# Optimization experiments

Measured on AMD Instinct MI355X. Metric: run time of the kernel, lower is better.

## Reference

```python
import jax, jax.numpy as jnp
import numpy as np

EPS = 1e-3  # tfa InstanceNormalization default epsilon
H = 4       # num_attention_heads


def _inorm(x, g, b, axes):
    # instance norm: normalize over the given (spatial) axes, affine per channel
    m = jnp.mean(x, axis=axes, keepdims=True)
    v = jnp.var(x, axis=axes, keepdims=True)
    return (x - m) * jax.lax.rsqrt(v + EPS) * g + b


def setup_inputs() -> dict:
    key = jax.random.key(0)
    ks = jax.random.split(key, 20)
    B, N, C, E = 1, 196, 480, 4  # batch, tokens, KV_size_C, embedding_channels
    d = {}
    for i, n in enumerate(['emb1', 'emb2', 'emb3', 'emb4']):
        d[n] = jax.random.normal(ks[i], (B, N, E), jnp.float32)
    d['emb_C'] = jax.random.normal(ks[4], (B, N, C), jnp.float32)
    for i, n in enumerate(['Wq_C', 'Wk_C', 'Wv_C']):
        d[n] = jax.random.normal(ks[5 + i], (C, C), jnp.float32) * 0.02
    for i, n in enumerate(['Wq1', 'Wq2', 'Wq3', 'Wq4', 'Wk', 'Wv', 'Wo1', 'Wo2', 'Wo3', 'Wo4']):
        d[n] = jax.random.normal(ks[8 + i], (E, E), jnp.float32) * 0.25
    d['g1'] = jnp.ones((), jnp.float32)   # psi1 gamma (single channel)
    d['b1'] = jnp.zeros((), jnp.float32)  # psi1 beta
    d['g2'] = jnp.ones((H,), jnp.float32)   # psi2 gamma (per head)
    d['b2'] = jnp.zeros((H,), jnp.float32)  # psi2 beta
    return d


def reference(emb1, emb2, emb3, emb4, emb_C, Wq_C, Wk_C, Wv_C,
              Wq1, Wq2, Wq3, Wq4, Wk, Wv, Wo1, Wo2, Wo3, Wo4,
              g1, b1, g2, b2):
    B, N, C = emb_C.shape
    # ---- channel attention over emb_C ----
    Qc = emb_C @ Wq_C
    Kc = emb_C @ Wk_C
    Vc = emb_C @ Wv_C
    attn = jnp.einsum('bnc,bnd->bcd', Qc, Kc)            # Q_C^T @ K_C  [B,C,C]
    attn = _inorm(attn, g1, b1, axes=(-2, -1))           # psi1: 1-channel instance norm
    sim = jax.nn.softmax(attn, axis=-1)                  # dropout inactive (inference)
    T_hat = jnp.einsum('bcd,bnd->bnc', sim, Vc)          # (sim @ V_C^T)^T  [B,N,C]
    # split into C//4 chunks of width 4 along channels, concat along tokens
    KV_S = T_hat.reshape(B, N, C // 4, 4).transpose(0, 2, 1, 3).reshape(B, (C // 4) * N, 4)

    def heads(x):  # [B,T,4] -> [B,H,T,1]
        return x.reshape(B, -1, H, 1).transpose(0, 2, 1, 3)

    K = heads(KV_S @ Wk)   # [B,H,M,1], M = N*C//4
    V = heads(KV_S @ Wv)
    gh = g2.reshape(1, H, 1, 1)
    bh = b2.reshape(1, H, 1, 1)

    def branch(emb, Wq, Wo):
        Q = heads(emb @ Wq)                                  # [B,H,Nq,1]
        a = jnp.einsum('bhqd,bhkd->bhqk', Q, K)              # [B,H,Nq,M]
        a = _inorm(a, gh, bh, axes=(-2, -1))                 # psi2: per-head instance norm
        a = jax.nn.softmax(a, axis=-1)
        c = jnp.einsum('bhqk,bhkd->bhqd', a, V)              # [B,H,Nq,1]
        c = c.transpose(0, 2, 1, 3).reshape(B, -1, H)        # [B,Nq,4] (= KV_size_S)
        return c @ Wo

    return (branch(emb1, Wq1, Wo1), branch(emb2, Wq2, Wo2),
            branch(emb3, Wq3, Wo3), branch(emb4, Wq4, Wo4))
```

## Files before the change

### kernel.cpp

```cpp
#include <hip/hip_runtime.h>
#include <hip/hip_bf16.h>
#include <math.h>

#define N_TOK 196
#define M_KV  23520
#define EPSN  1e-3f
#define LOG2E 1.44269504088896340736f

#define OFF_QC    0
#define OFF_KC    94080
#define OFF_VC    188160
#define OFF_ATTN  282240
#define OFF_KV    512640
#define OFF_SPART 700800
#define OFF_KPART 701056

__device__ __forceinline__ float fast_exp2(float x) {
#if __has_builtin(__builtin_amdgcn_exp2f)
    return __builtin_amdgcn_exp2f(x);
#else
    return exp2f(x);
#endif
}

#define GEMM_COMPUTE(AS, BS) \
    _Pragma("unroll") \
    for (int kk2 = 0; kk2 < 16; ++kk2) { \
        float4 av = *(const float4*)&AS[kk2][ty*4]; \
        float2 bv = *(const float2*)&BS[kk2][tx*2]; \
        a00 = fmaf(av.x, bv.x, a00); a01 = fmaf(av.x, bv.y, a01); \
        a10 = fmaf(av.y, bv.x, a10); a11 = fmaf(av.y, bv.y, a11); \
        a20 = fmaf(av.z, bv.x, a20); a21 = fmaf(av.z, bv.y, a21); \
        a30 = fmaf(av.w, bv.x, a30); a31 = fmaf(av.w, bv.y, a31); \
    }

#define COMBINE_ACCS(CMB) \
    if (kg == 1) { \
        CMB[ty*4+0][tx*2] = a00; CMB[ty*4+0][tx*2+1] = a01; \
        CMB[ty*4+1][tx*2] = a10; CMB[ty*4+1][tx*2+1] = a11; \
        CMB[ty*4+2][tx*2] = a20; CMB[ty*4+2][tx*2+1] = a21; \
        CMB[ty*4+3][tx*2] = a30; CMB[ty*4+3][tx*2+1] = a31; \
    } \
    __syncthreads(); \
    if (kg == 0) { \
        a00 += CMB[ty*4+0][tx*2]; a01 += CMB[ty*4+0][tx*2+1]; \
        a10 += CMB[ty*4+1][tx*2]; a11 += CMB[ty*4+1][tx*2+1]; \
        a20 += CMB[ty*4+2][tx*2]; a21 += CMB[ty*4+2][tx*2+1]; \
        a30 += CMB[ty*4+3][tx*2]; a31 += CMB[ty*4+3][tx*2+1]; \
    }

__global__ __launch_bounds__(512) void k_qkv(const float* __restrict__ embC,
                                             const float* __restrict__ Wq,
                                             const float* __restrict__ Wk,
                                             const float* __restrict__ Wv,
                                             float* __restrict__ ws) {
    int bid = blockIdx.x;
    int zi = bid / 60, rem = bid % 60;
    int m0 = (rem / 15) * 64, n0 = (rem % 15) * 32;
    const float* W = (zi == 0) ? Wq : (zi == 1 ? Wk : Wv);
    float* o = ws + zi * 94080;
    __shared__ float As[2][2][16][68];
    __shared__ float Bs[2][2][16][36];
    __shared__ float Cmb[64][33];
    int tid = threadIdx.x;
    int kg = tid >> 8, t = tid & 255;
    int ty = t >> 4, tx = t & 15;
    float a00=0,a01=0,a10=0,a11=0,a20=0,a21=0,a30=0,a31=0;
    const float4 z4 = make_float4(0,0,0,0);
    int mrow = t >> 2, kq = (t & 3) * 4;
    bool am = (m0 + mrow) < N_TOK;
    const float* aptr = embC + (m0 + mrow) * 480 + kg * 240 + kq;
    bool bact = t < 128;
    int kk = t >> 3, nq = (t & 7) * 4;
    const float* bptr = W + (kg * 240 + kk) * 480 + n0 + nq;
    const int NS = 15;
    float4 ra = am ? *(const float4*)(aptr) : z4;
    float4 rb = bact ? *(const float4*)(bptr) : z4;
    As[kg][0][kq+0][mrow]=ra.x; As[kg][0][kq+1][mrow]=ra.y;
    As[kg][0][kq+2][mrow]=ra.z; As[kg][0][kq+3][mrow]=ra.w;
    if (bact) *(float4*)&Bs[kg][0][kk][nq] = rb;
    ra = am ? *(const float4*)(aptr + 16) : z4;
    rb = bact ? *(const float4*)(bptr + 16*480) : z4;
    __syncthreads();
    for (int s = 0; s < NS; ++s) {
        int b = s & 1;
        float4 fa = z4, fb = z4;
        if (s + 2 < NS) {
            fa = am ? *(const float4*)(aptr + (s+2)*16) : z4;
            fb = bact ? *(const float4*)(bptr + (s+2)*16*480) : z4;
        }
        GEMM_COMPUTE(As[kg][b], Bs[kg][b]);
        if (s + 1 < NS) {
            int nb = b ^ 1;
            As[kg][nb][kq+0][mrow]=ra.x; As[kg][nb][kq+1][mrow]=ra.y;
            As[kg][nb][kq+2][mrow]=ra.z; As[kg][nb][kq+3][mrow]=ra.w;
            if (bact) *(float4*)&Bs[kg][nb][kk][nq] = rb;
        }
        __syncthreads();
        ra = fa; rb = fb;
    }
    COMBINE_ACCS(Cmb);
    if (kg == 0) {
        int m = m0 + ty*4, n = n0 + tx*2;
        if (m   < N_TOK) *(float2*)(o + (m  )*480 + n) = make_float2(a00, a01);
        if (m+1 < N_TOK) *(float2*)(o + (m+1)*480 + n) = make_float2(a10, a11);
        if (m+2 < N_TOK) *(float2*)(o + (m+2)*480 + n) = make_float2(a20, a21);
        if (m+3 < N_TOK) *(float2*)(o + (m+3)*480 + n) = make_float2(a30, a31);
    }
}

__global__ __launch_bounds__(512) void k_attn(const float* __restrict__ Qc,
                                              const float* __restrict__ Kc,
                                              float* __restrict__ attn,
                                              float* __restrict__ Spart) {
    __shared__ float As[2][2][16][68];
    __shared__ float Bs[2][2][16][36];
    __shared__ float Cmb[64][33];
    __shared__ float red[8][2];
    int tid = threadIdx.x;
    int kg = tid >> 8, t = tid & 255;
    int n0 = blockIdx.x * 32, m0 = blockIdx.y * 64;
    int ty = t >> 4, tx = t & 15;
    float a00=0,a01=0,a10=0,a11=0,a20=0,a21=0,a30=0,a31=0;
    const float4 z4 = make_float4(0,0,0,0);
    int kka = t >> 4, mq = (t & 15) * 4;
    bool amq = (m0 + mq) < 480;
    int kbase = kg * 112;
    const float* aptr = Qc + (kbase + kka) * 480 + m0 + mq;
    bool bact = t < 128;
    int kk = t >> 3, nq = (t & 7) * 4;
    const float* bptr = Kc + (kbase + kk) * 480 + n0 + nq;
    const int NS = 7;
    float4 ra = (amq && kbase + kka < N_TOK) ? *(const float4*)(aptr) : z4;
    float4 rb = (bact && kbase + kk < N_TOK) ? *(const float4*)(bptr) : z4;
    *(float4*)&As[kg][0][kka][mq] = ra;
    if (bact) *(float4*)&Bs[kg][0][kk][nq] = rb;
    ra = (amq && kbase + 16 + kka < N_TOK) ? *(const float4*)(aptr + 16*480) : z4;
    rb = (bact && kbase + 16 + kk < N_TOK) ? *(const float4*)(bptr + 16*480) : z4;
    __syncthreads();
    for (int s = 0; s < NS; ++s) {
        int b = s & 1;
        float4 fa = z4, fb = z4;
        if (s + 2 < NS) {
            int k0 = kbase + (s + 2) * 16;
            fa = (amq && k0 + kka < N_TOK) ? *(const float4*)(aptr + (s+2)*16*480) : z4;
            fb = (bact && k0 + kk < N_TOK) ? *(const float4*)(bptr + (s+2)*16*480) : z4;
        }
        GEMM_COMPUTE(As[kg][b], Bs[kg][b]);
        if (s + 1 < NS) {
            int nb = b ^ 1;
            *(float4*)&As[kg][nb][kka][mq] = ra;
            if (bact) *(float4*)&Bs[kg][nb][kk][nq] = rb;
        }
        __syncthreads();
        ra = fa; rb = fb;
    }
    COMBINE_ACCS(Cmb);
    float ls = 0.f, lq = 0.f;
    if (kg == 0) {
        int m = m0 + ty*4, n = n0 + tx*2;
        if (m   < 480) *(float2*)(attn + (m  )*480 + n) = make_float2(a00, a01);
        if (m+1 < 480) *(float2*)(attn + (m+1)*480 + n) = make_float2(a10, a11);
        if (m+2 < 480) *(float2*)(attn + (m+2)*480 + n) = make_float2(a20, a21);
        if (m+3 < 480) *(float2*)(attn + (m+3)*480 + n) = make_float2(a30, a31);
        ls = a00+a01+a10+a11+a20+a21+a30+a31;
        lq = a00*a00+a01*a01+a10*a10+a11*a11+a20*a20+a21*a21+a30*a30+a31*a31;
    }
    #pragma unroll
    for (int o = 32; o > 0; o >>= 1) { ls += __shfl_xor(ls, o, 64); lq += __shfl_xor(lq, o, 64); }
    int wid = tid >> 6, lane = tid & 63;
    if (lane == 0) { red[wid][0] = ls; red[wid][1] = lq; }
    __syncthreads();
    if (tid == 0) {
        int bid = blockIdx.y * gridDim.x + blockIdx.x;
        Spart[bid*2]   = red[0][0] + red[1][0] + red[2][0] + red[3][0];
        Spart[bid*2+1] = red[0][1] + red[1][1] + red[2][1] + red[3][1];
    }
}

__global__ __launch_bounds__(512) void k_thatkv(const float* __restrict__ Vc,
                                                const float* __restrict__ attn,
                                                const float* __restrict__ Spart,
                                                const float* __restrict__ g1,
                                                const float* __restrict__ Wk,
                                                const float* __restrict__ Wv,
                                                float2* __restrict__ KV,
                                                float* __restrict__ kpart) {
    __shared__ float As[2][2][16][68];
    __shared__ float Bs[2][2][16][36];
    __shared__ float red[8][16];
    __shared__ float colsum[32];
    __shared__ float Tile[64][33];
    int bid = blockIdx.x;
    int n0 = (bid % 15) * 32, m0 = (bid / 15) * 64;
    int tid = threadIdx.x;
    int kg = tid >> 8, t = tid & 255;
    int wid = tid >> 6, lane = tid & 63;
    if (tid < 32) colsum[tid] = 0.f;
    float ps = 0.f, pq = 0.f;
    if (tid < 120) { ps = Spart[tid*2]; pq = Spart[tid*2+1]; }
    #pragma unroll
    for (int o = 32; o > 0; o >>= 1) { ps += __shfl_xor(ps, o, 64); pq += __shfl_xor(pq, o, 64); }
    if (lane == 0) { red[wid][0] = ps; red[wid][1] = pq; }
    __syncthreads();
    float S = 0.f, SQ = 0.f;
    #pragma unroll
    for (int w = 0; w < 8; ++w) { S += red[w][0]; SQ += red[w][1]; }
    const float invCC = 1.f / (480.f * 480.f);
    float mean = S * invCC;
    float var  = SQ * invCC - mean * mean;
    float s2 = g1[0] * rsqrtf(var + EPSN) * LOG2E;
    int ty = t >> 4, tx = t & 15;
    float a00=0,a01=0,a10=0,a11=0,a20=0,a21=0,a30=0,a31=0;
    const float4 z4 = make_float4(0,0,0,0);
    int mrow = t >> 2, kq = (t & 3) * 4;
    bool am = (m0 + mrow) < N_TOK;
    const float* aptr = Vc + (m0 + mrow) * 480 + kg * 240 + kq;
    bool bact = t < 128;
    int nrow = t >> 2, bkq = (t & 3) * 4;
    const float* bptr = attn + (n0 + nrow) * 480 + kg * 240 + bkq;
    float bsum = 0.f;
    const int NS = 15;
    float4 ra = am ? *(const float4*)(aptr) : z4;
    float4 rb = bact ? *(const float4*)(bptr) : z4;
    As[kg][0][kq+0][mrow]=ra.x; As[kg][0][kq+1][mrow]=ra.y;
    As[kg][0][kq+2][mrow]=ra.z; As[kg][0][kq+3][mrow]=ra.w;
    if (bact) {
        float e0 = fast_exp2(s2 * rb.x), e1 = fast_exp2(s2 * rb.y);
        float e2 = fast_exp2(s2 * rb.z), e3 = fast_exp2(s2 * rb.w);
        Bs[kg][0][bkq+0][nrow] = e0; Bs[kg][0][bkq+1][nrow] = e1;
        Bs[kg][0][bkq+2][nrow] = e2; Bs[kg][0][bkq+3][nrow] = e3;
        bsum += e0 + e1 + e2 + e3;
    }
    ra = am ? *(const float4*)(aptr + 16) : z4;
    rb = bact ? *(const float4*)(bptr + 16) : z4;
    __syncthreads();
    for (int s = 0; s < NS; ++s) {
        int b = s & 1;
        float4 fa = z4, fb = z4;
        if (s + 2 < NS) {
            fa = am ? *(const float4*)(aptr + (s+2)*16) : z4;
            fb = bact ? *(const float4*)(bptr + (s+2)*16) : z4;
        }
        GEMM_COMPUTE(As[kg][b], Bs[kg][b]);
        if (s + 1 < NS) {
            int nb = b ^ 1;
            As[kg][nb][kq+0][mrow]=ra.x; As[kg][nb][kq+1][mrow]=ra.y;
            As[kg][nb][kq+2][mrow]=ra.z; As[kg][nb][kq+3][mrow]=ra.w;
            if (bact) {
                float e0 = fast_exp2(s2 * rb.x), e1 = fast_exp2(s2 * rb.y);
                float e2 = fast_exp2(s2 * rb.z), e3 = fast_exp2(s2 * rb.w);
                Bs[kg][nb][bkq+0][nrow] = e0; Bs[kg][nb][bkq+1][nrow] = e1;
                Bs[kg][nb][bkq+2][nrow] = e2; Bs[kg][nb][bkq+3][nrow] = e3;
                bsum += e0 + e1 + e2 + e3;
            }
        }
        __syncthreads();
        ra = fa; rb = fb;
    }
    if (bact) atomicAdd(&colsum[nrow], bsum);
    __syncthreads();
    if (tid < 32) colsum[tid] = 1.f / colsum[tid];
    int r0 = ty*4, cc = tx*2;
    if (kg == 1) {
        Tile[r0+0][cc] = a00; Tile[r0+0][cc+1] = a01;
        Tile[r0+1][cc] = a10; Tile[r0+1][cc+1] = a11;
        Tile[r0+2][cc] = a20; Tile[r0+2][cc+1] = a21;
        Tile[r0+3][cc] = a30; Tile[r0+3][cc+1] = a31;
    }
    __syncthreads();
    if (kg == 0) {
        float i0 = colsum[cc], i1 = colsum[cc+1];
        Tile[r0+0][cc] = (Tile[r0+0][cc] + a00) * i0; Tile[r0+0][cc+1] = (Tile[r0+0][cc+1] + a01) * i1;
        Tile[r0+1][cc] = (Tile[r0+1][cc] + a10) * i0; Tile[r0+1][cc+1] = (Tile[r0+1][cc+1] + a11) * i1;
        Tile[r0+2][cc] = (Tile[r0+2][cc] + a20) * i0; Tile[r0+2][cc+1] = (Tile[r0+2][cc+1] + a21) * i1;
        Tile[r0+3][cc] = (Tile[r0+3][cc] + a30) * i0; Tile[r0+3][cc+1] = (Tile[r0+3][cc+1] + a31) * i1;
    }
    __syncthreads();
    float su[4] = {0,0,0,0}, sq[4] = {0,0,0,0};
    {
        int e = tid;
        int tr = e >> 3, jj = e & 7;
        int tok = m0 + tr;
        bool act = tok < N_TOK;
        float c0 = Tile[tr][4*jj], c1 = Tile[tr][4*jj+1];
        float c2 = Tile[tr][4*jj+2], c3 = Tile[tr][4*jj+3];
        int m_kv = (n0/4 + jj) * 196 + tok;
        #pragma unroll
        for (int h = 0; h < 4; ++h) {
            float kh = c0*Wk[h] + c1*Wk[4+h] + c2*Wk[8+h] + c3*Wk[12+h];
            float vh = c0*Wv[h] + c1*Wv[4+h] + c2*Wv[8+h] + c3*Wv[12+h];
            if (act) {
                KV[h * M_KV + m_kv] = make_float2(kh, vh);
                su[h] += kh; sq[h] += kh * kh;
            }
        }
    }
    __syncthreads();
    #pragma unroll
    for (int h = 0; h < 4; ++h) {
        #pragma unroll
        for (int o = 32; o > 0; o >>= 1) {
            su[h] += __shfl_xor(su[h], o, 64);
            sq[h] += __shfl_xor(sq[h], o, 64);
        }
        if (lane == 0) { red[wid][h*2+0] = su[h]; red[wid][h*2+1] = sq[h]; }
    }
    __syncthreads();
    if (tid < 8) {
        int h = tid & 3, st = tid >> 2;
        float r = 0.f;
        #pragma unroll
        for (int w = 0; w < 8; ++w) r += red[w][h*2+st];
        kpart[st * 256 + h * 64 + bid] = r;
    }
}

#define QG 49
__global__ __launch_bounds__(1024) void k_branch(
        const float* __restrict__ emb1, const float* __restrict__ emb2,
        const float* __restrict__ emb3, const float* __restrict__ emb4,
        const float* __restrict__ Wq1, const float* __restrict__ Wq2,
        const float* __restrict__ Wq3, const float* __restrict__ Wq4,
        const float* __restrict__ g2v,
        const float2* __restrict__ KV, const float* __restrict__ kpart,
        const float* __restrict__ Wo1, const float* __restrict__ Wo2,
        const float* __restrict__ Wo3, const float* __restrict__ Wo4,
        float* __restrict__ out) {
    __shared__ float lsh[4][4][4];
    __shared__ float ash[4][4][4];
    int tid = threadIdx.x;
    int w = tid >> 6, lane = tid & 63;
    int h = w >> 2, p = w & 3;
    int bid = blockIdx.x;
    int i = bid / QG, qg = bid % QG;
    const float* emb = (i == 0) ? emb1 : (i == 1) ? emb2 : (i == 2) ? emb3 : emb4;
    const float* Wq  = (i == 0) ? Wq1 : (i == 1) ? Wq2 : (i == 2) ? Wq3 : Wq4;
    float wq0 = Wq[h], wq1 = Wq[4+h], wq2 = Wq[8+h], wq3 = Wq[12+h];
    float s = 0.f, s2 = 0.f;
    #pragma unroll
    for (int r = 0; r < 4; ++r) {
        int t = lane + r * 64;
        if (t < N_TOK) {
            float Q = emb[t*4]*wq0 + emb[t*4+1]*wq1 + emb[t*4+2]*wq2 + emb[t*4+3]*wq3;
            s += Q; s2 += Q * Q;
        }
    }
    float ks = 0.f, kq2 = 0.f;
    if (lane < 60) {
        ks  = kpart[0*256 + h*64 + lane];
        kq2 = kpart[1*256 + h*64 + lane];
    }
    #pragma unroll
    for (int o = 32; o > 0; o >>= 1) {
        s += __shfl_xor(s, o, 64); s2 += __shfl_xor(s2, o, 64);
        ks += __shfl_xor(ks, o, 64); kq2 += __shfl_xor(kq2, o, 64);
    }
    float Qbar = s * (1.f/196.f), Q2bar = s2 * (1.f/196.f);
    float Kbar = ks * (1.f/(float)M_KV), K2bar = kq2 * (1.f/(float)M_KV);
    float mu = Qbar * Kbar;
    float var = Q2bar * K2bar - mu * mu;
    float sc = g2v[h] * rsqrtf(var + EPSN);
    float B2[4];
    #pragma unroll
    for (int j = 0; j < 4; ++j) {
        int q = qg * 4 + j;
        float Qj = emb[q*4]*wq0 + emb[q*4+1]*wq1 + emb[q*4+2]*wq2 + emb[q*4+3]*wq3;
        B2[j] = Qj * sc * LOG2E;
    }
    const float4* kv4 = (const float4*)(KV + h * M_KV);
    const int KQ = M_KV / 8;
    int kstart = p * KQ, kendq = kstart + KQ;
    float l[4] = {0,0,0,0};
    float a[4] = {0,0,0,0};
#define PROC8(P) { \
        _Pragma("unroll") \
        for (int j = 0; j < 4; ++j) { \
            float x = fast_exp2(B2[j] * P.x); \
            l[j] += x; a[j] = fmaf(x, P.y, a[j]); \
            float y = fast_exp2(B2[j] * P.z); \
            l[j] += y; a[j] = fmaf(y, P.w, a[j]); \
        } }
    int k4 = kstart + lane;
    for (; k4 + 192 < kendq; k4 += 256) {
        float4 p0 = kv4[k4], p1 = kv4[k4+64], p2 = kv4[k4+128], p3 = kv4[k4+192];
        PROC8(p0); PROC8(p1); PROC8(p2); PROC8(p3);
    }
    for (; k4 < kendq; k4 += 64) { float4 pv = kv4[k4]; PROC8(pv); }
#undef PROC8
    #pragma unroll
    for (int j = 0; j < 4; ++j) {
        float lv = l[j], av = a[j];
        #pragma unroll
        for (int o = 32; o > 0; o >>= 1) { lv += __shfl_xor(lv, o, 64); av += __shfl_xor(av, o, 64); }
        if (lane == 0) { lsh[h][p][j] = lv; ash[h][p][j] = av; }
    }
    __syncthreads();
    if (tid < 4) {
        const float* Wo = (i == 0) ? Wo1 : (i == 1) ? Wo2 : (i == 2) ? Wo3 : Wo4;
        int j = tid;
        float c[4];
        #pragma unroll
        for (int hh = 0; hh < 4; ++hh) {
            float L = lsh[hh][0][j] + lsh[hh][1][j] + lsh[hh][2][j] + lsh[hh][3][j];
            float A = ash[hh][0][j] + ash[hh][1][j] + ash[hh][2][j] + ash[hh][3][j];
            c[hh] = A / L;
        }
        float4 o;
        o.x = c[0]*Wo[0] + c[1]*Wo[4] + c[2]*Wo[8]  + c[3]*Wo[12];
        o.y = c[0]*Wo[1] + c[1]*Wo[5] + c[2]*Wo[9]  + c[3]*Wo[13];
        o.z = c[0]*Wo[2] + c[1]*Wo[6] + c[2]*Wo[10] + c[3]*Wo[14];
        o.w = c[0]*Wo[3] + c[1]*Wo[7] + c[2]*Wo[11] + c[3]*Wo[15];
        *(float4*)(out + i * 784 + (qg * 4 + j) * 4) = o;
    }
}

extern "C" void kernel_launch(void* const* d_in, const int* in_sizes, int n_in,
                              void* d_out, int out_size, void* d_ws, size_t ws_size,
                              hipStream_t stream) {
    const float* emb1 = (const float*)d_in[0];
    const float* emb2 = (const float*)d_in[1];
    const float* emb3 = (const float*)d_in[2];
    const float* emb4 = (const float*)d_in[3];
    const float* embC = (const float*)d_in[4];
    const float* WqC  = (const float*)d_in[5];
    const float* WkC  = (const float*)d_in[6];
    const float* WvC  = (const float*)d_in[7];
    const float* Wq1  = (const float*)d_in[8];
    const float* Wq2  = (const float*)d_in[9];
    const float* Wq3  = (const float*)d_in[10];
    const float* Wq4  = (const float*)d_in[11];
    const float* Wk   = (const float*)d_in[12];
    const float* Wv   = (const float*)d_in[13];
    const float* Wo1  = (const float*)d_in[14];
    const float* Wo2  = (const float*)d_in[15];
    const float* Wo3  = (const float*)d_in[16];
    const float* Wo4  = (const float*)d_in[17];
    const float* g1   = (const float*)d_in[18];
    const float* g2   = (const float*)d_in[20];
    float* ws = (float*)d_ws;
    float* out = (float*)d_out;

    k_qkv<<<180, 512, 0, stream>>>(embC, WqC, WkC, WvC, ws);
    k_attn<<<dim3(15, 8), 512, 0, stream>>>(ws + OFF_QC, ws + OFF_KC,
                                            ws + OFF_ATTN, ws + OFF_SPART);
    k_thatkv<<<60, 512, 0, stream>>>(ws + OFF_VC, ws + OFF_ATTN, ws + OFF_SPART, g1,
                                     Wk, Wv, (float2*)(ws + OFF_KV), ws + OFF_KPART);
    k_branch<<<4 * QG, 1024, 0, stream>>>(emb1, emb2, emb3, emb4,
                                          Wq1, Wq2, Wq3, Wq4, g2,
                                          (const float2*)(ws + OFF_KV), ws + OFF_KPART,
                                          Wo1, Wo2, Wo3, Wo4, out);
}
```

Before: 64.87 us.

## Fuse four kernels into one persistent kernel with grid-wide atomic barriers

Measured after the change: 95.21 us. +46.8%, slower.

```diff
diff --git a/kernel.cpp b/kernel.cpp
--- a/kernel.cpp
+++ b/kernel.cpp
@@ -6,6 +6,7 @@
 #define M_KV  23520
 #define EPSN  1e-3f
 #define LOG2E 1.44269504088896340736f
+#define NB    256
 
 #define OFF_QC    0
 #define OFF_KC    94080
@@ -14,6 +15,7 @@
 #define OFF_KV    512640
 #define OFF_SPART 700800
 #define OFF_KPART 701056
+#define OFF_SYNC  702080
 
 __device__ __forceinline__ float fast_exp2(float x) {
 #if __has_builtin(__builtin_amdgcn_exp2f)
@@ -21,6 +23,31 @@
 #else
     return exp2f(x);
 #endif
+}
+
+__device__ __forceinline__ void gsync(unsigned* sy, int phase, int bid) {
+    __syncthreads();
+    if (threadIdx.x == 0) {
+        __builtin_amdgcn_fence(__ATOMIC_RELEASE, "agent");
+        unsigned* grp  = sy + phase * 16 + (bid >> 4);
+        unsigned* glob = sy + 128 + phase;
+        unsigned* go   = sy + 144 + phase * 16;
+        if (__hip_atomic_fetch_add(grp, 1u, __ATOMIC_RELAXED, __HIP_MEMORY_SCOPE_AGENT) == 15u) {
+            if (__hip_atomic_fetch_add(glob, 1u, __ATOMIC_RELAXED, __HIP_MEMORY_SCOPE_AGENT) == 15u) {
+                __hip_atomic_store(go, 1u, __ATOMIC_RELAXED, __HIP_MEMORY_SCOPE_AGENT);
+            }
+        }
+        int it = 0;
+        while (__hip_atomic_load(go, __ATOMIC_RELAXED, __HIP_MEMORY_SCOPE_AGENT) == 0u) {
+            if (it < 2)      __builtin_amdgcn_s_sleep(1);
+            else if (it < 4) __builtin_amdgcn_s_sleep(4);
+            else if (it < 8) __builtin_amdgcn_s_sleep(16);
+            else             __builtin_amdgcn_s_sleep(32);
+            ++it;
+        }
+        __builtin_amdgcn_fence(__ATOMIC_ACQUIRE, "agent");
+    }
+    __syncthreads();
 }
 
 #define GEMM_COMPUTE(AS, BS) \
@@ -34,345 +61,341 @@
         a30 = fmaf(av.w, bv.x, a30); a31 = fmaf(av.w, bv.y, a31); \
     }
 
-#define COMBINE_ACCS(CMB) \
-    if (kg == 1) { \
-        CMB[ty*4+0][tx*2] = a00; CMB[ty*4+0][tx*2+1] = a01; \
-        CMB[ty*4+1][tx*2] = a10; CMB[ty*4+1][tx*2+1] = a11; \
-        CMB[ty*4+2][tx*2] = a20; CMB[ty*4+2][tx*2+1] = a21; \
-        CMB[ty*4+3][tx*2] = a30; CMB[ty*4+3][tx*2+1] = a31; \
-    } \
-    __syncthreads(); \
-    if (kg == 0) { \
-        a00 += CMB[ty*4+0][tx*2]; a01 += CMB[ty*4+0][tx*2+1]; \
-        a10 += CMB[ty*4+1][tx*2]; a11 += CMB[ty*4+1][tx*2+1]; \
-        a20 += CMB[ty*4+2][tx*2]; a21 += CMB[ty*4+2][tx*2+1]; \
-        a30 += CMB[ty*4+3][tx*2]; a31 += CMB[ty*4+3][tx*2+1]; \
-    }
-
-__global__ __launch_bounds__(512) void k_qkv(const float* __restrict__ embC,
-                                             const float* __restrict__ Wq,
-                                             const float* __restrict__ Wk,
-                                             const float* __restrict__ Wv,
-                                             float* __restrict__ ws) {
-    int bid = blockIdx.x;
-    int zi = bid / 60, rem = bid % 60;
-    int m0 = (rem / 15) * 64, n0 = (rem % 15) * 32;
-    const float* W = (zi == 0) ? Wq : (zi == 1 ? Wk : Wv);
-    float* o = ws + zi * 94080;
+__global__ __launch_bounds__(512) void k_fused(
+        const float* __restrict__ emb1, const float* __restrict__ emb2,
+        const float* __restrict__ emb3, const float* __restrict__ emb4,
+        const float* __restrict__ embC,
+        const float* __restrict__ WqC, const float* __restrict__ WkC, const float* __restrict__ WvC,
+        const float* __restrict__ Wq1, const float* __restrict__ Wq2,
+        const float* __restrict__ Wq3, const float* __restrict__ Wq4,
+        const float* __restrict__ Wk,  const float* __restrict__ Wv,
+        const float* __restrict__ Wo1, const float* __restrict__ Wo2,
+        const float* __restrict__ Wo3, const float* __restrict__ Wo4,
+        const float* __restrict__ g1,  const float* __restrict__ g2v,
+        float* __restrict__ ws, float* __restrict__ out) {
     __shared__ float As[2][2][16][68];
     __shared__ float Bs[2][2][16][36];
     __shared__ float Cmb[64][33];
-    int tid = threadIdx.x;
-    int kg = tid >> 8, t = tid & 255;
-    int ty = t >> 4, tx = t & 15;
-    float a00=0,a01=0,a10=0,a11=0,a20=0,a21=0,a30=0,a31=0;
-    const float4 z4 = make_float4(0,0,0,0);
-    int mrow = t >> 2, kq = (t & 3) * 4;
-    bool am = (m0 + mrow) < N_TOK;
-    const float* aptr = embC + (m0 + mrow) * 480 + kg * 240 + kq;
-    bool bact = t < 128;
-    int kk = t >> 3, nq = (t & 7) * 4;
-    const float* bptr = W + (kg * 240 + kk) * 480 + n0 + nq;
-    const int NS = 15;
-    float4 ra = am ? *(const float4*)(aptr) : z4;
-    float4 rb = bact ? *(const float4*)(bptr) : z4;
-    As[kg][0][kq+0][mrow]=ra.x; As[kg][0][kq+1][mrow]=ra.y;
-    As[kg][0][kq+2][mrow]=ra.z; As[kg][0][kq+3][mrow]=ra.w;
-    if (bact) *(float4*)&Bs[kg][0][kk][nq] = rb;
-    ra = am ? *(const float4*)(aptr + 16) : z4;
-    rb = bact ? *(const float4*)(bptr + 16*480) : z4;
-    __syncthreads();
-    for (int s = 0; s < NS; ++s) {
-        int b = s & 1;
-        float4 fa = z4, fb = z4;
-        if (s + 2 < NS) {
-            fa = am ? *(const float4*)(aptr + (s+2)*16) : z4;
-            fb = bact ? *(const float4*)(bptr + (s+2)*16*480) : z4;
-        }
-        GEMM_COMPUTE(As[kg][b], Bs[kg][b]);
-        if (s + 1 < NS) {
-            int nb = b ^ 1;
-            As[kg][nb][kq+0][mrow]=ra.x; As[kg][nb][kq+1][mrow]=ra.y;
-            As[kg][nb][kq+2][mrow]=ra.z; As[kg][nb][kq+3][mrow]=ra.w;
-            if (bact) *(float4*)&Bs[kg][nb][kk][nq] = rb;
-        }
-        __syncthreads();
-        ra = fa; rb = fb;
-    }
-    COMBINE_ACCS(Cmb);
-    if (kg == 0) {
-        int m = m0 + ty*4, n = n0 + tx*2;
-        if (m   < N_TOK) *(float2*)(o + (m  )*480 + n) = make_float2(a00, a01);
-        if (m+1 < N_TOK) *(float2*)(o + (m+1)*480 + n) = make_float2(a10, a11);
-        if (m+2 < N_TOK) *(float2*)(o + (m+2)*480 + n) = make_float2(a20, a21);
-        if (m+3 < N_TOK) *(float2*)(o + (m+3)*480 + n) = make_float2(a30, a31);
-    }
-}
-
-__global__ __launch_bounds__(512) void k_attn(const float* __restrict__ Qc,
-                                              const float* __restrict__ Kc,
-                                              float* __restrict__ attn,
-                                              float* __restrict__ Spart) {
-    __shared__ float As[2][2][16][68];
-    __shared__ float Bs[2][2][16][36];
-    __shared__ float Cmb[64][33];
-    __shared__ float red[8][2];
-    int tid = threadIdx.x;
-    int kg = tid >> 8, t = tid & 255;
-    int n0 = blockIdx.x * 32, m0 = blockIdx.y * 64;
-    int ty = t >> 4, tx = t & 15;
-    float a00=0,a01=0,a10=0,a11=0,a20=0,a21=0,a30=0,a31=0;
-    const float4 z4 = make_float4(0,0,0,0);
-    int kka = t >> 4, mq = (t & 15) * 4;
-    bool amq = (m0 + mq) < 480;
-    int kbase = kg * 112;
-    const float* aptr = Qc + (kbase + kka) * 480 + m0 + mq;
-    bool bact = t < 128;
-    int kk = t >> 3, nq = (t & 7) * 4;
-    const float* bptr = Kc + (kbase + kk) * 480 + n0 + nq;
-    const int NS = 7;
-    float4 ra = (amq && kbase + kka < N_TOK) ? *(const float4*)(aptr) : z4;
-    float4 rb = (bact && kbase + kk < N_TOK) ? *(const float4*)(bptr) : z4;
-    *(float4*)&As[kg][0][kka][mq] = ra;
-    if (bact) *(float4*)&Bs[kg][0][kk][nq] = rb;
-    ra = (amq && kbase + 16 + kka < N_TOK) ? *(const float4*)(aptr + 16*480) : z4;
-    rb = (bact && kbase + 16 + kk < N_TOK) ? *(const float4*)(bptr + 16*480) : z4;
-    __syncthreads();
-    for (int s = 0; s < NS; ++s) {
-        int b = s & 1;
-        float4 fa = z4, fb = z4;
-        if (s + 2 < NS) {
-            int k0 = kbase + (s + 2) * 16;
-            fa = (amq && k0 + kka < N_TOK) ? *(const float4*)(aptr + (s+2)*16*480) : z4;
-            fb = (bact && k0 + kk < N_TOK) ? *(const float4*)(bptr + (s+2)*16*480) : z4;
-        }
-        GEMM_COMPUTE(As[kg][b], Bs[kg][b]);
-        if (s + 1 < NS) {
-            int nb = b ^ 1;
-            *(float4*)&As[kg][nb][kka][mq] = ra;
-            if (bact) *(float4*)&Bs[kg][nb][kk][nq] = rb;
-        }
-        __syncthreads();
-        ra = fa; rb = fb;
-    }
-    COMBINE_ACCS(Cmb);
-    float ls = 0.f, lq = 0.f;
-    if (kg == 0) {
-        int m = m0 + ty*4, n = n0 + tx*2;
-        if (m   < 480) *(float2*)(attn + (m  )*480 + n) = make_float2(a00, a01);
-        if (m+1 < 480) *(float2*)(attn + (m+1)*480 + n) = make_float2(a10, a11);
-        if (m+2 < 480) *(float2*)(attn + (m+2)*480 + n) = make_float2(a20, a21);
-        if (m+3 < 480) *(float2*)(attn + (m+3)*480 + n) = make_float2(a30, a31);
-        ls = a00+a01+a10+a11+a20+a21+a30+a31;
-        lq = a00*a00+a01*a01+a10*a10+a11*a11+a20*a20+a21*a21+a30*a30+a31*a31;
-    }
-    #pragma unroll
-    for (int o = 32; o > 0; o >>= 1) { ls += __shfl_xor(ls, o, 64); lq += __shfl_xor(lq, o, 64); }
-    int wid = tid >> 6, lane = tid & 63;
-    if (lane == 0) { red[wid][0] = ls; red[wid][1] = lq; }
-    __syncthreads();
-    if (tid == 0) {
-        int bid = blockIdx.y * gridDim.x + blockIdx.x;
-        Spart[bid*2]   = red[0][0] + red[1][0] + red[2][0] + red[3][0];
-        Spart[bid*2+1] = red[0][1] + red[1][1] + red[2][1] + red[3][1];
-    }
-}
-
-__global__ __launch_bounds__(512) void k_thatkv(const float* __restrict__ Vc,
-                                                const float* __restrict__ attn,
-                                                const float* __restrict__ Spart,
-                                                const float* __restrict__ g1,
-                                                const float* __restrict__ Wk,
-                                                const float* __restrict__ Wv,
-                                                float2* __restrict__ KV,
-                                                float* __restrict__ kpart) {
-    __shared__ float As[2][2][16][68];
-    __shared__ float Bs[2][2][16][36];
+    __shared__ float Tile[64][33];
     __shared__ float red[8][16];
     __shared__ float colsum[32];
-    __shared__ float Tile[64][33];
-    int bid = blockIdx.x;
-    int n0 = (bid % 15) * 32, m0 = (bid / 15) * 64;
-    int tid = threadIdx.x;
-    int kg = tid >> 8, t = tid & 255;
-    int wid = tid >> 6, lane = tid & 63;
-    if (tid < 32) colsum[tid] = 0.f;
-    float ps = 0.f, pq = 0.f;
-    if (tid < 120) { ps = Spart[tid*2]; pq = Spart[tid*2+1]; }
-    #pragma unroll
-    for (int o = 32; o > 0; o >>= 1) { ps += __shfl_xor(ps, o, 64); pq += __shfl_xor(pq, o, 64); }
-    if (lane == 0) { red[wid][0] = ps; red[wid][1] = pq; }
-    __syncthreads();
-    float S = 0.f, SQ = 0.f;
-    #pragma unroll
-    for (int w = 0; w < 8; ++w) { S += red[w][0]; SQ += red[w][1]; }
-    const float invCC = 1.f / (480.f * 480.f);
-    float mean = S * invCC;
-    float var  = SQ * invCC - mean * mean;
-    float s2 = g1[0] * rsqrtf(var + EPSN) * LOG2E;
-    int ty = t >> 4, tx = t & 15;
-    float a00=0,a01=0,a10=0,a11=0,a20=0,a21=0,a30=0,a31=0;
+    __shared__ float lsh[4][2][4];
+    __shared__ float ash[4][2][4];
+
+    unsigned* sy = (unsigned*)(ws + OFF_SYNC);
+    const int bid = blockIdx.x;
+    const int tid = threadIdx.x;
+    const int kg = tid >> 8, t = tid & 255;
+    const int wid = tid >> 6, lane = tid & 63;
     const float4 z4 = make_float4(0,0,0,0);
-    int mrow = t >> 2, kq = (t & 3) * 4;
-    bool am = (m0 + mrow) < N_TOK;
-    const float* aptr = Vc + (m0 + mrow) * 480 + kg * 240 + kq;
-    bool bact = t < 128;
-    int nrow = t >> 2, bkq = (t & 3) * 4;
-    const float* bptr = attn + (n0 + nrow) * 480 + kg * 240 + bkq;
-    float bsum = 0.f;
-    const int NS = 15;
-    float4 ra = am ? *(const float4*)(aptr) : z4;
-    float4 rb = bact ? *(const float4*)(bptr) : z4;
-    As[kg][0][kq+0][mrow]=ra.x; As[kg][0][kq+1][mrow]=ra.y;
-    As[kg][0][kq+2][mrow]=ra.z; As[kg][0][kq+3][mrow]=ra.w;
-    if (bact) {
-        float e0 = fast_exp2(s2 * rb.x), e1 = fast_exp2(s2 * rb.y);
-        float e2 = fast_exp2(s2 * rb.z), e3 = fast_exp2(s2 * rb.w);
-        Bs[kg][0][bkq+0][nrow] = e0; Bs[kg][0][bkq+1][nrow] = e1;
-        Bs[kg][0][bkq+2][nrow] = e2; Bs[kg][0][bkq+3][nrow] = e3;
-        bsum += e0 + e1 + e2 + e3;
-    }
-    ra = am ? *(const float4*)(aptr + 16) : z4;
-    rb = bact ? *(const float4*)(bptr + 16) : z4;
-    __syncthreads();
-    for (int s = 0; s < NS; ++s) {
-        int b = s & 1;
-        float4 fa = z4, fb = z4;
-        if (s + 2 < NS) {
-            fa = am ? *(const float4*)(aptr + (s+2)*16) : z4;
-            fb = bact ? *(const float4*)(bptr + (s+2)*16) : z4;
-        }
-        GEMM_COMPUTE(As[kg][b], Bs[kg][b]);
-        if (s + 1 < NS) {
-            int nb = b ^ 1;
-            As[kg][nb][kq+0][mrow]=ra.x; As[kg][nb][kq+1][mrow]=ra.y;
-            As[kg][nb][kq+2][mrow]=ra.z; As[kg][nb][kq+3][mrow]=ra.w;
-            if (bact) {
-                float e0 = fast_exp2(s2 * rb.x), e1 = fast_exp2(s2 * rb.y);
-                float e2 = fast_exp2(s2 * rb.z), e3 = fast_exp2(s2 * rb.w);
-                Bs[kg][nb][bkq+0][nrow] = e0; Bs[kg][nb][bkq+1][nrow] = e1;
-                Bs[kg][nb][bkq+2][nrow] = e2; Bs[kg][nb][bkq+3][nrow] = e3;
-                bsum += e0 + e1 + e2 + e3;
-            }
-        }
-        __syncthreads();
-        ra = fa; rb = fb;
-    }
-    if (bact) atomicAdd(&colsum[nrow], bsum);
-    __syncthreads();
-    if (tid < 32) colsum[tid] = 1.f / colsum[tid];
-    int r0 = ty*4, cc = tx*2;
-    if (kg == 1) {
-        Tile[r0+0][cc] = a00; Tile[r0+0][cc+1] = a01;
-        Tile[r0+1][cc] = a10; Tile[r0+1][cc+1] = a11;
-        Tile[r0+2][cc] = a20; Tile[r0+2][cc+1] = a21;
-        Tile[r0+3][cc] = a30; Tile[r0+3][cc+1] = a31;
-    }
-    __syncthreads();
-    if (kg == 0) {
-        float i0 = colsum[cc], i1 = colsum[cc+1];
-        Tile[r0+0][cc] = (Tile[r0+0][cc] + a00) * i0; Tile[r0+0][cc+1] = (Tile[r0+0][cc+1] + a01) * i1;
-        Tile[r0+1][cc] = (Tile[r0+1][cc] + a10) * i0; Tile[r0+1][cc+1] = (Tile[r0+1][cc+1] + a11) * i1;
-        Tile[r0+2][cc] = (Tile[r0+2][cc] + a20) * i0; Tile[r0+2][cc+1] = (Tile[r0+2][cc+1] + a21) * i1;
-        Tile[r0+3][cc] = (Tile[r0+3][cc] + a30) * i0; Tile[r0+3][cc+1] = (Tile[r0+3][cc+1] + a31) * i1;
-    }
-    __syncthreads();
-    float su[4] = {0,0,0,0}, sq[4] = {0,0,0,0};
-    {
-        int e = tid;
-        int tr = e >> 3, jj = e & 7;
-        int tok = m0 + tr;
-        bool act = tok < N_TOK;
-        float c0 = Tile[tr][4*jj], c1 = Tile[tr][4*jj+1];
-        float c2 = Tile[tr][4*jj+2], c3 = Tile[tr][4*jj+3];
-        int m_kv = (n0/4 + jj) * 196 + tok;
+
+    if (bid < 180) {
+        int zi = bid / 60, rem = bid % 60;
+        int m0 = (rem / 15) * 64, n0 = (rem % 15) * 32;
+        const float* W = (zi == 0) ? WqC : (zi == 1 ? WkC : WvC);
+        float* o = ws + zi * 94080;
+        int ty = t >> 4, tx = t & 15;
+        float a00=0,a01=0,a10=0,a11=0,a20=0,a21=0,a30=0,a31=0;
+        int mrow = t >> 2, kq = (t & 3) * 4;
+        bool am = (m0 + mrow) < N_TOK;
+        const float* aptr = embC + (m0 + mrow) * 480 + kg * 240 + kq;
+        bool bact = t < 128;
+        int kk = t >> 3, nq = (t & 7) * 4;
+        const float* bptr = W + (kg * 240 + kk) * 480 + n0 + nq;
+        const int NS = 15;
+        float4 ra = am ? *(const float4*)(aptr) : z4;
+        float4 rb = bact ? *(const float4*)(bptr) : z4;
+        As[kg][0][kq+0][mrow]=ra.x; As[kg][0][kq+1][mrow]=ra.y;
+        As[kg][0][kq+2][mrow]=ra.z; As[kg][0][kq+3][mrow]=ra.w;
+        if (bact) *(float4*)&Bs[kg][0][kk][nq] = rb;
+        ra = am ? *(const float4*)(aptr + 16) : z4;
+        rb = bact ? *(const float4*)(bptr + 16*480) : z4;
+        __syncthreads();
+        for (int s = 0; s < NS; ++s) {
+            int b = s & 1;
+            float4 fa = z4, fb = z4;
+            if (s + 2 < NS) {
+                fa = am ? *(const float4*)(aptr + (s+2)*16) : z4;
+                fb = bact ? *(const float4*)(bptr + (s+2)*16*480) : z4;
+            }
+            GEMM_COMPUTE(As[kg][b], Bs[kg][b]);
+            if (s + 1 < NS) {
+                int nb = b ^ 1;
+                As[kg][nb][kq+0][mrow]=ra.x; As[kg][nb][kq+1][mrow]=ra.y;
+                As[kg][nb][kq+2][mrow]=ra.z; As[kg][nb][kq+3][mrow]=ra.w;
+                if (bact) *(float4*)&Bs[kg][nb][kk][nq] = rb;
+            }
+            __syncthreads();
+            ra = fa; rb = fb;
+        }
+        if (kg == 1) {
+            Cmb[ty*4+0][tx*2] = a00; Cmb[ty*4+0][tx*2+1] = a01;
+            Cmb[ty*4+1][tx*2] = a10; Cmb[ty*4+1][tx*2+1] = a11;
+            Cmb[ty*4+2][tx*2] = a20; Cmb[ty*4+2][tx*2+1] = a21;
+            Cmb[ty*4+3][tx*2] = a30; Cmb[ty*4+3][tx*2+1] = a31;
+        }
+        __syncthreads();
+        if (kg == 0) {
+            a00 += Cmb[ty*4+0][tx*2]; a01 += Cmb[ty*4+0][tx*2+1];
+            a10 += Cmb[ty*4+1][tx*2]; a11 += Cmb[ty*4+1][tx*2+1];
+            a20 += Cmb[ty*4+2][tx*2]; a21 += Cmb[ty*4+2][tx*2+1];
+            a30 += Cmb[ty*4+3][tx*2]; a31 += Cmb[ty*4+3][tx*2+1];
+            int m = m0 + ty*4, n = n0 + tx*2;
+            if (m   < N_TOK) *(float2*)(o + (m  )*480 + n) = make_float2(a00, a01);
+            if (m+1 < N_TOK) *(float2*)(o + (m+1)*480 + n) = make_float2(a10, a11);
+            if (m+2 < N_TOK) *(float2*)(o + (m+2)*480 + n) = make_float2(a20, a21);
+            if (m+3 < N_TOK) *(float2*)(o + (m+3)*480 + n) = make_float2(a30, a31);
+        }
+    }
+    gsync(sy, 0, bid);
+
+    if (bid < 120) {
+        const float* Qc = ws + OFF_QC;
+        const float* Kc = ws + OFF_KC;
+        float* attn = ws + OFF_ATTN;
+        float* Spart = ws + OFF_SPART;
+        int n0 = (bid % 15) * 32, m0 = (bid / 15) * 64;
+        int ty = t >> 4, tx = t & 15;
+        float a00=0,a01=0,a10=0,a11=0,a20=0,a21=0,a30=0,a31=0;
+        int kka = t >> 4, mq = (t & 15) * 4;
+        bool amq = (m0 + mq) < 480;
+        int kbase = kg * 112;
+        const float* aptr = Qc + (kbase + kka) * 480 + m0 + mq;
+        bool bact = t < 128;
+        int kk = t >> 3, nq = (t & 7) * 4;
+        const float* bptr = Kc + (kbase + kk) * 480 + n0 + nq;
+        const int NS = 7;
+        float4 ra = (amq && kbase + kka < N_TOK) ? *(const float4*)(aptr) : z4;
+        float4 rb = (bact && kbase + kk < N_TOK) ? *(const float4*)(bptr) : z4;
+        *(float4*)&As[kg][0][kka][mq] = ra;
+        if (bact) *(float4*)&Bs[kg][0][kk][nq] = rb;
+        ra = (amq && kbase + 16 + kka < N_TOK) ? *(const float4*)(aptr + 16*480) : z4;
+        rb = (bact && kbase + 16 + kk < N_TOK) ? *(const float4*)(bptr + 16*480) : z4;
+        __syncthreads();
+        for (int s = 0; s < NS; ++s) {
+            int b = s & 1;
+            float4 fa = z4, fb = z4;
+            if (s + 2 < NS) {
+                int k0 = kbase + (s + 2) * 16;
+                fa = (amq && k0 + kka < N_TOK) ? *(const float4*)(aptr + (s+2)*16*480) : z4;
+                fb = (bact && k0 + kk < N_TOK) ? *(const float4*)(bptr + (s+2)*16*480) : z4;
+            }
+            GEMM_COMPUTE(As[kg][b], Bs[kg][b]);
+            if (s + 1 < NS) {
+                int nb = b ^ 1;
+                *(float4*)&As[kg][nb][kka][mq] = ra;
+                if (bact) *(float4*)&Bs[kg][nb][kk][nq] = rb;
+            }
+            __syncthreads();
+            ra = fa; rb = fb;
+        }
+        if (kg == 1) {
+            Cmb[ty*4+0][tx*2] = a00; Cmb[ty*4+0][tx*2+1] = a01;
+            Cmb[ty*4+1][tx*2] = a10; Cmb[ty*4+1][tx*2+1] = a11;
+            Cmb[ty*4+2][tx*2] = a20; Cmb[ty*4+2][tx*2+1] = a21;
+            Cmb[ty*4+3][tx*2] = a30; Cmb[ty*4+3][tx*2+1] = a31;
+        }
+        __syncthreads();
+        float ls = 0.f, lq = 0.f;
+        if (kg == 0) {
+            a00 += Cmb[ty*4+0][tx*2]; a01 += Cmb[ty*4+0][tx*2+1];
+            a10 += Cmb[ty*4+1][tx*2]; a11 += Cmb[ty*4+1][tx*2+1];
+            a20 += Cmb[ty*4+2][tx*2]; a21 += Cmb[ty*4+2][tx*2+1];
+            a30 += Cmb[ty*4+3][tx*2]; a31 += Cmb[ty*4+3][tx*2+1];
+            int m = m0 + ty*4, n = n0 + tx*2;
+            if (m   < 480) *(float2*)(attn + (m  )*480 + n) = make_float2(a00, a01);
+            if (m+1 < 480) *(float2*)(attn + (m+1)*480 + n) = make_float2(a10, a11);
+            if (m+2 < 480) *(float2*)(attn + (m+2)*480 + n) = make_float2(a20, a21);
+            if (m+3 < 480) *(float2*)(attn + (m+3)*480 + n) = make_float2(a30, a31);
+            ls = a00+a01+a10+a11+a20+a21+a30+a31;
+            lq = a00*a00+a01*a01+a10*a10+a11*a11+a20*a20+a21*a21+a30*a30+a31*a31;
+        }
+        #pragma unroll
+        for (int o = 32; o > 0; o >>= 1) { ls += __shfl_xor(ls, o, 64); lq += __shfl_xor(lq, o, 64); }
+        if (lane == 0) { red[wid][0] = ls; red[wid][1] = lq; }
+        __syncthreads();
+        if (tid == 0) {
+            float S = 0.f, SQ = 0.f;
+            #pragma unroll
+            for (int w = 0; w < 8; ++w) { S += red[w][0]; SQ += red[w][1]; }
+            Spart[bid*2]   = S;
+            Spart[bid*2+1] = SQ;
+        }
+    }
+    gsync(sy, 1, bid);
+
+    if (bid < 60) {
+        const float* Vc = ws + OFF_VC;
+        const float* attn = ws + OFF_ATTN;
+        const float* Spart = ws + OFF_SPART;
+        float2* KV = (float2*)(ws + OFF_KV);
+        float* kpart = ws + OFF_KPART;
+        int n0 = (bid % 15) * 32, m0 = (bid / 15) * 64;
+        if (tid < 32) colsum[tid] = 0.f;
+        float ps = 0.f, pq = 0.f;
+        if (tid < 120) { ps = Spart[tid*2]; pq = Spart[tid*2+1]; }
+        #pragma unroll
+        for (int o = 32; o > 0; o >>= 1) { ps += __shfl_xor(ps, o, 64); pq += __shfl_xor(pq, o, 64); }
+        if (lane == 0) { red[wid][0] = ps; red[wid][1] = pq; }
+        __syncthreads();
+        float S = 0.f, SQ = 0.f;
+        #pragma unroll
+        for (int w = 0; w < 8; ++w) { S += red[w][0]; SQ += red[w][1]; }
+        const float invCC = 1.f / (480.f * 480.f);
+        float mean = S * invCC;
+        float var  = SQ * invCC - mean * mean;
+        float s2 = g1[0] * rsqrtf(var + EPSN) * LOG2E;
+        int ty = t >> 4, tx = t & 15;
+        float a00=0,a01=0,a10=0,a11=0,a20=0,a21=0,a30=0,a31=0;
+        int mrow = t >> 2, kq = (t & 3) * 4;
+        bool am = (m0 + mrow) < N_TOK;
+        const float* aptr = Vc + (m0 + mrow) * 480 + kg * 240 + kq;
+        bool bact = t < 128;
+        int nrow = t >> 2, bkq = (t & 3) * 4;
+        const float* bptr = attn + (n0 + nrow) * 480 + kg * 240 + bkq;
+        float bsum = 0.f;
+        const int NS = 15;
+        float4 ra = am ? *(const float4*)(aptr) : z4;
+        float4 rb = bact ? *(const float4*)(bptr) : z4;
+        As[kg][0][kq+0][mrow]=ra.x; As[kg][0][kq+1][mrow]=ra.y;
+        As[kg][0][kq+2][mrow]=ra.z; As[kg][0][kq+3][mrow]=ra.w;
+        if (bact) {
+            float e0 = fast_exp2(s2 * rb.x), e1 = fast_exp2(s2 * rb.y);
+            float e2 = fast_exp2(s2 * rb.z), e3 = fast_exp2(s2 * rb.w);
+            Bs[kg][0][bkq+0][nrow] = e0; Bs[kg][0][bkq+1][nrow] = e1;
+            Bs[kg][0][bkq+2][nrow] = e2; Bs[kg][0][bkq+3][nrow] = e3;
+            bsum += e0 + e1 + e2 + e3;
+        }
+        ra = am ? *(const float4*)(aptr + 16) : z4;
+        rb = bact ? *(const float4*)(bptr + 16) : z4;
+        __syncthreads();
+        for (int s = 0; s < NS; ++s) {
+            int b = s & 1;
+            float4 fa = z4, fb = z4;
+            if (s + 2 < NS) {
+                fa = am ? *(const float4*)(aptr + (s+2)*16) : z4;
+                fb = bact ? *(const float4*)(bptr + (s+2)*16) : z4;
+            }
+            GEMM_COMPUTE(As[kg][b], Bs[kg][b]);
+            if (s + 1 < NS) {
+                int nb = b ^ 1;
+                As[kg][nb][kq+0][mrow]=ra.x; As[kg][nb][kq+1][mrow]=ra.y;
+                As[kg][nb][kq+2][mrow]=ra.z; As[kg][nb][kq+3][mrow]=ra.w;
+                if (bact) {
+                    float e0 = fast_exp2(s2 * rb.x), e1 = fast_exp2(s2 * rb.y);
+                    float e2 = fast_exp2(s2 * rb.z), e3 = fast_exp2(s2 * rb.w);
+                    Bs[kg][nb][bkq+0][nrow] = e0; Bs[kg][nb][bkq+1][nrow] = e1;
+                    Bs[kg][nb][bkq+2][nrow] = e2; Bs[kg][nb][bkq+3][nrow] = e3;
+                    bsum += e0 + e1 + e2 + e3;
+                }
+            }
+            __syncthreads();
+            ra = fa; rb = fb;
+        }
+        if (bact) atomicAdd(&colsum[nrow], bsum);
+        int r0 = ty*4, cc = tx*2;
+        if (kg == 1) {
+            Tile[r0+0][cc] = a00; Tile[r0+0][cc+1] = a01;
+            Tile[r0+1][cc] = a10; Tile[r0+1][cc+1] = a11;
+            Tile[r0+2][cc] = a20; Tile[r0+2][cc+1] = a21;
+            Tile[r0+3][cc] = a30; Tile[r0+3][cc+1] = a31;
+        }
+        __syncthreads();
+        if (tid < 32) colsum[tid] = 1.f / colsum[tid];
+        __syncthreads();
+        if (kg == 0) {
+            float i0 = colsum[cc], i1 = colsum[cc+1];
+            Tile[r0+0][cc] = (Tile[r0+0][cc] + a00) * i0; Tile[r0+0][cc+1] = (Tile[r0+0][cc+1] + a01) * i1;
+            Tile[r0+1][cc] = (Tile[r0+1][cc] + a10) * i0; Tile[r0+1][cc+1] = (Tile[r0+1][cc+1] + a11) * i1;
+            Tile[r0+2][cc] = (Tile[r0+2][cc] + a20) * i0; Tile[r0+2][cc+1] = (Tile[r0+2][cc+1] + a21) * i1;
+            Tile[r0+3][cc] = (Tile[r0+3][cc] + a30) * i0; Tile[r0+3][cc+1] = (Tile[r0+3][cc+1] + a31) * i1;
+        }
+        __syncthreads();
+        float su[4] = {0,0,0,0}, sq[4] = {0,0,0,0};
+        {
+            int e = tid;
+            int tr = e >> 3, jj = e & 7;
+            int tok = m0 + tr;
+            bool act = tok < N_TOK;
+            float c0 = Tile[tr][4*jj], c1 = Tile[tr][4*jj+1];
+            float c2 = Tile[tr][4*jj+2], c3 = Tile[tr][4*jj+3];
+            int m_kv = (n0/4 + jj) * 196 + tok;
+            #pragma unroll
+            for (int h = 0; h < 4; ++h) {
+                float kh = c0*Wk[h] + c1*Wk[4+h] + c2*Wk[8+h] + c3*Wk[12+h];
+                float vh = c0*Wv[h] + c1*Wv[4+h] + c2*Wv[8+h] + c3*Wv[12+h];
+                if (act) {
+                    KV[h * M_KV + m_kv] = make_float2(kh, vh);
+                    su[h] += kh; sq[h] += kh * kh;
+                }
+            }
+        }
+        __syncthreads();
         #pragma unroll
         for (int h = 0; h < 4; ++h) {
-            float kh = c0*Wk[h] + c1*Wk[4+h] + c2*Wk[8+h] + c3*Wk[12+h];
-            float vh = c0*Wv[h] + c1*Wv[4+h] + c2*Wv[8+h] + c3*Wv[12+h];
-            if (act) {
-                KV[h * M_KV + m_kv] = make_float2(kh, vh);
-                su[h] += kh; sq[h] += kh * kh;
-            }
-        }
-    }
-    __syncthreads();
-    #pragma unroll
-    for (int h = 0; h < 4; ++h) {
+            #pragma unroll
+            for (int o = 32; o > 0; o >>= 1) {
+                su[h] += __shfl_xor(su[h], o, 64);
+                sq[h] += __shfl_xor(sq[h], o, 64);
+            }
+            if (lane == 0) { red[wid][h*2+0] = su[h]; red[wid][h*2+1] = sq[h]; }
+        }
+        __syncthreads();
+        if (tid < 8) {
+            int h = tid & 3, st = tid >> 2;
+            float r = 0.f;
+            #pragma unroll
+            for (int w = 0; w < 8; ++w) r += red[w][h*2+st];
+            kpart[st * 256 + h * 64 + bid] = r;
+        }
+    }
+    gsync(sy, 2, bid);
+
+    if (bid < 196) {
+        const float2* KV = (const float2*)(ws + OFF_KV);
+        const float* kpart = ws + OFF_KPART;
+        int w = wid;
+        int h = w >> 1, p = w & 1;
+        int i = bid / 49, qg = bid % 49;
+        const float* emb = (i == 0) ? emb1 : (i == 1) ? emb2 : (i == 2) ? emb3 : emb4;
+        const float* Wq  = (i == 0) ? Wq1 : (i == 1) ? Wq2 : (i == 2) ? Wq3 : Wq4;
+        float wq0 = Wq[h], wq1 = Wq[4+h], wq2 = Wq[8+h], wq3 = Wq[12+h];
+        float s = 0.f, s2 = 0.f;
+        #pragma unroll
+        for (int r = 0; r < 4; ++r) {
+            int tt = lane + r * 64;
+            if (tt < N_TOK) {
+                float Q = emb[tt*4]*wq0 + emb[tt*4+1]*wq1 + emb[tt*4+2]*wq2 + emb[tt*4+3]*wq3;
+                s += Q; s2 += Q * Q;
+            }
+        }
+        float ks = 0.f, kq2 = 0.f;
+        if (lane < 60) {
+            ks  = kpart[0*256 + h*64 + lane];
+            kq2 = kpart[1*256 + h*64 + lane];
+        }
         #pragma unroll
         for (int o = 32; o > 0; o >>= 1) {
-            su[h] += __shfl_xor(su[h], o, 64);
-            sq[h] += __shfl_xor(sq[h], o, 64);
-        }
-        if (lane == 0) { red[wid][h*2+0] = su[h]; red[wid][h*2+1] = sq[h]; }
-    }
-    __syncthreads();
-    if (tid < 8) {
-        int h = tid & 3, st = tid >> 2;
-        float r = 0.f;
-        #pragma unroll
-        for (int w = 0; w < 8; ++w) r += red[w][h*2+st];
-        kpart[st * 256 + h * 64 + bid] = r;
-    }
-}
-
-#define QG 49
-__global__ __launch_bounds__(1024) void k_branch(
-        const float* __restrict__ emb1, const float* __restrict__ emb2,
-        const float* __restrict__ emb3, const float* __restrict__ emb4,
-        const float* __restrict__ Wq1, const float* __restrict__ Wq2,
-        const float* __restrict__ Wq3, const float* __restrict__ Wq4,
-        const float* __restrict__ g2v,
-        const float2* __restrict__ KV, const float* __restrict__ kpart,
-        const float* __restrict__ Wo1, const float* __restrict__ Wo2,
-        const float* __restrict__ Wo3, const float* __restrict__ Wo4,
-        float* __restrict__ out) {
-    __shared__ float lsh[4][4][4];
-    __shared__ float ash[4][4][4];
-    int tid = threadIdx.x;
-    int w = tid >> 6, lane = tid & 63;
-    int h = w >> 2, p = w & 3;
-    int bid = blockIdx.x;
-    int i = bid / QG, qg = bid % QG;
-    const float* emb = (i == 0) ? emb1 : (i == 1) ? emb2 : (i == 2) ? emb3 : emb4;
-    const float* Wq  = (i == 0) ? Wq1 : (i == 1) ? Wq2 : (i == 2) ? Wq3 : Wq4;
-    float wq0 = Wq[h], wq1 = Wq[4+h], wq2 = Wq[8+h], wq3 = Wq[12+h];
-    float s = 0.f, s2 = 0.f;
-    #pragma unroll
-    for (int r = 0; r < 4; ++r) {
-        int t = lane + r * 64;
-        if (t < N_TOK) {
-            float Q = emb[t*4]*wq0 + emb[t*4+1]*wq1 + emb[t*4+2]*wq2 + emb[t*4+3]*wq3;
-            s += Q; s2 += Q * Q;
-        }
-    }
-    float ks = 0.f, kq2 = 0.f;
-    if (lane < 60) {
-        ks  = kpart[0*256 + h*64 + lane];
-        kq2 = kpart[1*256 + h*64 + lane];
-    }
-    #pragma unroll
-    for (int o = 32; o > 0; o >>= 1) {
-        s += __shfl_xor(s, o, 64); s2 += __shfl_xor(s2, o, 64);
-        ks += __shfl_xor(ks, o, 64); kq2 += __shfl_xor(kq2, o, 64);
-    }
-    float Qbar = s * (1.f/196.f), Q2bar = s2 * (1.f/196.f);
-    float Kbar = ks * (1.f/(float)M_KV), K2bar = kq2 * (1.f/(float)M_KV);
-    float mu = Qbar * Kbar;
-    float var = Q2bar * K2bar - mu * mu;
-    float sc = g2v[h] * rsqrtf(var + EPSN);
-    float B2[4];
-    #pragma unroll
-    for (int j = 0; j < 4; ++j) {
-        int q = qg * 4 + j;
-        float Qj = emb[q*4]*wq0 + emb[q*4+1]*wq1 + emb[q*4+2]*wq2 + emb[q*4+3]*wq3;
-        B2[j] = Qj * sc * LOG2E;
-    }
-    const float4* kv4 = (const float4*)(KV + h * M_KV);
-    const int KQ = M_KV / 8;
-    int kstart = p * KQ, kendq = kstart + KQ;
-    float l[4] = {0,0,0,0};
-    float a[4] = {0,0,0,0};
+            s += __shfl_xor(s, o, 64); s2 += __shfl_xor(s2, o, 64);
+            ks += __shfl_xor(ks, o, 64); kq2 += __shfl_xor(kq2, o, 64);
+        }
+        float Qbar = s * (1.f/196.f), Q2bar = s2 * (1.f/196.f);
+        float Kbar = ks * (1.f/(float)M_KV), K2bar = kq2 * (1.f/(float)M_KV);
+        float mu = Qbar * Kbar;
+        float var = Q2bar * K2bar - mu * mu;
+        float sc = g2v[h] * rsqrtf(var + EPSN);
+        float B2[4];
+        #pragma unroll
+        for (int j = 0; j < 4; ++j) {
+            int q = qg * 4 + j;
+            float Qj = emb[q*4]*wq0 + emb[q*4+1]*wq1 + emb[q*4+2]*wq2 + emb[q*4+3]*wq3;
+            B2[j] = Qj * sc * LOG2E;
+        }
+        const float4* kv4 = (const float4*)(KV + h * M_KV);
+        const int KH = M_KV / 4;
+        int kstart = p * KH, kendq = kstart + KH;
+        float l[4] = {0,0,0,0};
+        float a[4] = {0,0,0,0};
 #define PROC8(P) { \
         _Pragma("unroll") \
         for (int j = 0; j < 4; ++j) { \
@@ -381,37 +404,38 @@
             float y = fast_exp2(B2[j] * P.z); \
             l[j] += y; a[j] = fmaf(y, P.w, a[j]); \
         } }
-    int k4 = kstart + lane;
-    for (; k4 + 192 < kendq; k4 += 256) {
-        float4 p0 = kv4[k4], p1 = kv4[k4+64], p2 = kv4[k4+128], p3 = kv4[k4+192];
-        PROC8(p0); PROC8(p1); PROC8(p2); PROC8(p3);
-    }
-    for (; k4 < kendq; k4 += 64) { float4 pv = kv4[k4]; PROC8(pv); }
+        int k4 = kstart + lane;
+        for (; k4 + 192 < kendq; k4 += 256) {
+            float4 p0 = kv4[k4], p1 = kv4[k4+64], p2 = kv4[k4+128], p3 = kv4[k4+192];
+            PROC8(p0); PROC8(p1); PROC8(p2); PROC8(p3);
+        }
+        for (; k4 < kendq; k4 += 64) { float4 pv = kv4[k4]; PROC8(pv); }
 #undef PROC8
-    #pragma unroll
-    for (int j = 0; j < 4; ++j) {
-        float lv = l[j], av = a[j];
-        #pragma unroll
-        for (int o = 32; o > 0; o >>= 1) { lv += __shfl_xor(lv, o, 64); av += __shfl_xor(av, o, 64); }
-        if (lane == 0) { lsh[h][p][j] = lv; ash[h][p][j] = av; }
-    }
-    __syncthreads();
-    if (tid < 4) {
-        const float* Wo = (i == 0) ? Wo1 : (i == 1) ? Wo2 : (i == 2) ? Wo3 : Wo4;
-        int j = tid;
-        float c[4];
-        #pragma unroll
-        for (int hh = 0; hh < 4; ++hh) {
-            float L = lsh[hh][0][j] + lsh[hh][1][j] + lsh[hh][2][j] + lsh[hh][3][j];
-            float A = ash[hh][0][j] + ash[hh][1][j] + ash[hh][2][j] + ash[hh][3][j];
-            c[hh] = A / L;
-        }
-        float4 o;
-        o.x = c[0]*Wo[0] + c[1]*Wo[4] + c[2]*Wo[8]  + c[3]*Wo[12];
-        o.y = c[0]*Wo[1] + c[1]*Wo[5] + c[2]*Wo[9]  + c[3]*Wo[13];
-        o.z = c[0]*Wo[2] + c[1]*Wo[6] + c[2]*Wo[10] + c[3]*Wo[14];
-        o.w = c[0]*Wo[3] + c[1]*Wo[7] + c[2]*Wo[11] + c[3]*Wo[15];
-        *(float4*)(out + i * 784 + (qg * 4 + j) * 4) = o;
+        #pragma unroll
+        for (int j = 0; j < 4; ++j) {
+            float lv = l[j], av = a[j];
+            #pragma unroll
+            for (int o = 32; o > 0; o >>= 1) { lv += __shfl_xor(lv, o, 64); av += __shfl_xor(av, o, 64); }
+            if (lane == 0) { lsh[h][p][j] = lv; ash[h][p][j] = av; }
+        }
+        __syncthreads();
+        if (tid < 4) {
+            const float* Wo = (i == 0) ? Wo1 : (i == 1) ? Wo2 : (i == 2) ? Wo3 : Wo4;
+            int j = tid;
+            float c[4];
+            #pragma unroll
+            for (int hh = 0; hh < 4; ++hh) {
+                float L = lsh[hh][0][j] + lsh[hh][1][j];
+                float A = ash[hh][0][j] + ash[hh][1][j];
+                c[hh] = A / L;
+            }
+            float4 o;
+            o.x = c[0]*Wo[0] + c[1]*Wo[4] + c[2]*Wo[8]  + c[3]*Wo[12];
+            o.y = c[0]*Wo[1] + c[1]*Wo[5] + c[2]*Wo[9]  + c[3]*Wo[13];
+            o.z = c[0]*Wo[2] + c[1]*Wo[6] + c[2]*Wo[10] + c[3]*Wo[14];
+            o.w = c[0]*Wo[3] + c[1]*Wo[7] + c[2]*Wo[11] + c[3]*Wo[15];
+            *(float4*)(out + i * 784 + (qg * 4 + j) * 4) = o;
+        }
     }
 }
 
@@ -441,13 +465,10 @@
     float* ws = (float*)d_ws;
     float* out = (float*)d_out;
 
-    k_qkv<<<180, 512, 0, stream>>>(embC, WqC, WkC, WvC, ws);
-    k_attn<<<dim3(15, 8), 512, 0, stream>>>(ws + OFF_QC, ws + OFF_KC,
-                                            ws + OFF_ATTN, ws + OFF_SPART);
-    k_thatkv<<<60, 512, 0, stream>>>(ws + OFF_VC, ws + OFF_ATTN, ws + OFF_SPART, g1,
-                                     Wk, Wv, (float2*)(ws + OFF_KV), ws + OFF_KPART);
-    k_branch<<<4 * QG, 1024, 0, stream>>>(emb1, emb2, emb3, emb4,
-                                          Wq1, Wq2, Wq3, Wq4, g2,
-                                          (const float2*)(ws + OFF_KV), ws + OFF_KPART,
-                                          Wo1, Wo2, Wo3, Wo4, out);
+    hipMemsetAsync(ws + OFF_SYNC, 0, 272 * sizeof(unsigned), stream);
+
+    k_fused<<<NB, 512, 0, stream>>>(emb1, emb2, emb3, emb4, embC,
+                                    WqC, WkC, WvC,
+                                    Wq1, Wq2, Wq3, Wq4, Wk, Wv,
+                                    Wo1, Wo2, Wo3, Wo4, g1, g2, ws, out);
 }
```
